# Kernel tuning notes

Measured on AMD Instinct MI355X. Metric: run time of the kernel, lower is better.

Reference implementation:

```python
import jax, jax.numpy as jnp
import numpy as np

N_NODES = 100000
N_EDGES = 3200000
IN_DIM = 256
HIDDEN = 128
OUT_DIM = 64


def setup_inputs() -> dict:
    key = jax.random.key(0)
    k = jax.random.split(key, 6)
    x = jax.random.normal(k[0], (N_NODES, IN_DIM), dtype=jnp.float32)
    adj_vals = jax.random.uniform(k[1], (N_EDGES,), dtype=jnp.float32)
    # glorot init as in the original
    s1 = np.sqrt(6.0 / (IN_DIM + HIDDEN)).astype(np.float32)
    s2 = np.sqrt(6.0 / (HIDDEN + OUT_DIM)).astype(np.float32)
    w1 = jax.random.uniform(k[2], (IN_DIM, HIDDEN), dtype=jnp.float32, minval=-s1, maxval=s1)
    w2 = jax.random.uniform(k[3], (HIDDEN, OUT_DIM), dtype=jnp.float32, minval=-s2, maxval=s2)
    edge_src = jax.random.randint(k[4], (N_EDGES,), 0, N_NODES, dtype=jnp.int32)
    edge_dst = jax.random.randint(k[5], (N_EDGES,), 0, N_NODES, dtype=jnp.int32)
    return {"x": x, "adj_vals": adj_vals, "w1": w1, "w2": w2,
            "edge_src": edge_src, "edge_dst": edge_dst}


def _spmm(adj_vals, edge_src, edge_dst, h, n_nodes):
    """Sparse adjacency (COO) times dense matrix: out[d] = sum_e vals[e]*h[src[e]]."""
    msgs = adj_vals[:, None] * h[edge_src]  # [E, D] gather + scale
    return jax.ops.segment_sum(msgs, edge_dst, num_segments=n_nodes)


def reference(x, adj_vals, w1, w2, edge_src, edge_dst):
    # Layer 1: pre_sup = X @ W1; support = A @ pre_sup; relu
    h = jax.nn.relu(_spmm(adj_vals, edge_src, edge_dst, x @ w1, N_NODES))
    # Layer 2: identity activation -> logits
    logits = _spmm(adj_vals, edge_src, edge_dst, h @ w2, N_NODES)
    return logits
```

## Files before the change

### kernel.cpp

```cpp
#include <hip/hip_runtime.h>

#define N_NODES 100000
#define N_EDGES 3200000
#define IN_DIM 256
#define HIDDEN 128
#define OUT_DIM 64

#define NBUCK 782
#define CHUNK 5120
#define BCAP 6144

typedef unsigned int uint32;
typedef unsigned short ushort16;

typedef short short8 __attribute__((ext_vector_type(8)));
typedef float f32x4 __attribute__((ext_vector_type(4)));

__device__ __forceinline__ ushort16 f2bf(float f) {
    uint32 u = __float_as_uint(f);
    u += 0x7fffu + ((u >> 16) & 1u);
    return (ushort16)(u >> 16);
}

__device__ __forceinline__ void splitbf(float f, unsigned short& hi, unsigned short& lo) {
    uint32 u = __float_as_uint(f);
    uint32 r = u + 0x7fffu + ((u >> 16) & 1u);
    hi = (unsigned short)(r >> 16);
    float hf = __uint_as_float((r >> 16) << 16);
    float res = f - hf;
    uint32 v = __float_as_uint(res);
    lo = (unsigned short)((v + 0x7fffu + ((v >> 16) & 1u)) >> 16);
}


__global__ __launch_bounds__(256)
void hist_bucket(const int* __restrict__ edst, int* __restrict__ bcnt, int E) {
    __shared__ int h[NBUCK];
    for (int b = threadIdx.x; b < NBUCK; b += 256) h[b] = 0;
    __syncthreads();
    for (int i = blockIdx.x * 256 + threadIdx.x; i < E; i += gridDim.x * 256)
        atomicAdd(&h[edst[i] >> 7], 1);
    __syncthreads();
    for (int b = threadIdx.x; b < NBUCK; b += 256) {
        int c = h[b];
        if (c) atomicAdd(&bcnt[b], c);
    }
}


__global__ __launch_bounds__(256)
void bucket_scan(const int* __restrict__ bcnt, int* __restrict__ bptr,
                 int* __restrict__ cursor, int* __restrict__ row_ptr, int E) {
    __shared__ int st[256];
    int tid = threadIdx.x;
    int v4[4];
    int s0 = 0;
#pragma unroll
    for (int k = 0; k < 4; k++) {
        int b = tid * 4 + k;
        v4[k] = (b < NBUCK) ? bcnt[b] : 0;
        s0 += v4[k];
    }
    st[tid] = s0;
    __syncthreads();
    for (int off = 1; off < 256; off <<= 1) {
        int t = (tid >= off) ? st[tid - off] : 0;
        __syncthreads();
        st[tid] += t;
        __syncthreads();
    }
    int run = st[tid] - s0;
#pragma unroll
    for (int k = 0; k < 4; k++) {
        int b = tid * 4 + k;
        if (b < NBUCK) { bptr[b] = run; cursor[b] = run; }
        run += v4[k];
    }
    if (tid == 255) bptr[NBUCK] = run;
    if (tid == 0) row_ptr[N_NODES] = E;
}


__global__ __launch_bounds__(256)
void partition_kernel(const int* __restrict__ esrc, const int* __restrict__ edst,
                      const float* __restrict__ evals, int* __restrict__ cursor,
                      int2* __restrict__ part, int E) {
    __shared__ int hist[NBUCK];
    __shared__ int basepos[NBUCK];
    __shared__ int st[256];
    __shared__ unsigned short sbb[CHUNK];
    __shared__ int2 sbp[CHUNK];
    int tid = threadIdx.x;
    long base = (long)blockIdx.x * CHUNK;
    int cnt = (int)min((long)CHUNK, (long)E - base);

    for (int b = tid; b < NBUCK; b += 256) hist[b] = 0;
    __syncthreads();
    for (int j = tid; j < cnt; j += 256)
        atomicAdd(&hist[edst[base + j] >> 7], 1);
    __syncthreads();

    int v4[4];
    int s0 = 0;
#pragma unroll
    for (int k = 0; k < 4; k++) {
        int b = tid * 4 + k;
        v4[k] = (b < NBUCK) ? hist[b] : 0;
        s0 += v4[k];
    }
    st[tid] = s0;
    __syncthreads();
    for (int off = 1; off < 256; off <<= 1) {
        int t = (tid >= off) ? st[tid - off] : 0;
        __syncthreads();
        st[tid] += t;
        __syncthreads();
    }
    int run = st[tid] - s0;
#pragma unroll
    for (int k = 0; k < 4; k++) {
        int b = tid * 4 + k;
        if (b < NBUCK) {
            int gbase = (v4[k] > 0) ? atomicAdd(&cursor[b], v4[k]) : 0;
            basepos[b] = gbase - run;
            hist[b] = run;
        }
        run += v4[k];
    }
    __syncthreads();

    for (int j = tid; j < cnt; j += 256) {
        int d = edst[base + j];
        int b = d >> 7;
        int pos = atomicAdd(&hist[b], 1);
        sbb[pos] = (unsigned short)b;
        sbp[pos] = make_int2(esrc[base + j] | ((d & 127) << 17),
                             __float_as_int(evals[base + j]));
    }
    __syncthreads();

    for (int j = tid; j < cnt; j += 256) {
        int b = sbb[j];
        part[basepos[b] + j] = sbp[j];
    }
}


__global__ __launch_bounds__(256)
void bucket_to_csr(const int* __restrict__ bptr, int2* __restrict__ part,
                   int* __restrict__ row_ptr) {
    __shared__ int2 se[BCAP];
    __shared__ int rcnt[128];
    __shared__ int rcur[128];
    int tid = threadIdx.x;
    int b = blockIdx.x;
    int s = bptr[b], e = bptr[b + 1];
    int cnt = min(e - s, BCAP);

    if (tid < 128) rcnt[tid] = 0;
    __syncthreads();
    for (int j = tid; j < cnt; j += 256) {
        int2 p = part[s + j];
        se[j] = p;
        atomicAdd(&rcnt[p.x >> 17], 1);
    }
    __syncthreads();

    int v = (tid < 128) ? rcnt[tid] : 0;
    if (tid < 128) rcur[tid] = v;
    __syncthreads();
    for (int off = 1; off < 128; off <<= 1) {
        int t = 0;
        if (tid < 128 && tid >= off) t = rcur[tid - off];
        __syncthreads();
        if (tid < 128 && tid >= off) rcur[tid] += t;
        __syncthreads();
    }
    if (tid < 128) {
        int excl = rcur[tid] - v;
        rcur[tid] = excl;
        int row = b * 128 + tid;
        if (row < N_NODES) row_ptr[row] = s + excl;
    }
    __syncthreads();

    for (int j = tid; j < cnt; j += 256) {
        int2 p = se[j];
        int r = p.x >> 17;
        int pos = atomicAdd(&rcur[r], 1);
        part[s + pos] = make_int2(p.x & 0x1FFFF, p.y);
    }
}


__global__ __launch_bounds__(256)
void splitw_kernel(const float* __restrict__ w1, const float* __restrict__ w2,
                   ushort16* __restrict__ w1t_hi, ushort16* __restrict__ w1t_lo,
                   ushort16* __restrict__ w2t_hi, ushort16* __restrict__ w2t_lo) {
    int g = blockIdx.x * 256 + threadIdx.x;
    if (g < IN_DIM * HIDDEN) {
        int k = g / HIDDEN, n = g % HIDDEN;
        unsigned short h, l;
        splitbf(w1[g], h, l);
        w1t_hi[n * IN_DIM + k] = h;
        w1t_lo[n * IN_DIM + k] = l;
    } else {
        int g2 = g - IN_DIM * HIDDEN;
        if (g2 < HIDDEN * OUT_DIM) {
            int k = g2 / OUT_DIM, n = g2 % OUT_DIM;
            unsigned short h, l;
            splitbf(w2[g2], h, l);
            w2t_hi[n * HIDDEN + k] = h;
            w2t_lo[n * HIDDEN + k] = l;
        }
    }
}


template <int K, int BN>
__launch_bounds__(256)
__global__ void gemm_mfma(const float* __restrict__ A,
                          const ushort16* __restrict__ Bt_hi,
                          const ushort16* __restrict__ Bt_lo,
                          ushort16* __restrict__ C, int M) {
    constexpr int BM = 128, BK = 64;
    constexpr int NF = BN / 32;
    __shared__ __align__(16) unsigned short Ah[BM * BK];
    __shared__ __align__(16) unsigned short Al[BM * BK];

    int tid = threadIdx.x;
    int wid = tid >> 6, lane = tid & 63;
    int wr = wid >> 1, wc = wid & 1;
    int rowBase = blockIdx.x * BM;
    int r = lane & 15, kg = lane >> 4;
    int swzmask = (lane & 7) << 4;

    f32x4 zero = {0.f, 0.f, 0.f, 0.f};
    f32x4 acc[4][NF];
#pragma unroll
    for (int m = 0; m < 4; m++)
#pragma unroll
        for (int n = 0; n < NF; n++) acc[m][n] = zero;

    int sk4 = (tid & 15) * 4;
    int sm0 = tid >> 4;

    for (int k0 = 0; k0 < K; k0 += BK) {
#pragma unroll
        for (int i = 0; i < 8; i++) {
            int m = sm0 + i * 16;
            int row = rowBase + m;
            float4 f = make_float4(0.f, 0.f, 0.f, 0.f);
            if (row < M) f = *(const float4*)(A + (size_t)row * K + k0 + sk4);
            ushort4 h, l;
            splitbf(f.x, h.x, l.x);
            splitbf(f.y, h.y, l.y);
            splitbf(f.z, h.z, l.z);
            splitbf(f.w, h.w, l.w);
            int bo = (m * BK + sk4) * 2;
            int swz = bo ^ ((m & 7) << 4);
            *(ushort4*)((char*)Ah + swz) = h;
            *(ushort4*)((char*)Al + swz) = l;
        }
        __syncthreads();

#pragma unroll
        for (int kk = 0; kk < BK / 32; kk++) {
            short8 ah[4], al[4];
            int abase = (wr * 64 + r) * (BK * 2) + kk * 64 + kg * 16;
#pragma unroll
            for (int m = 0; m < 4; m++) {
                int swz = (abase + m * (16 * BK * 2)) ^ swzmask;
                ah[m] = *(const short8*)((const char*)Ah + swz);
                al[m] = *(const short8*)((const char*)Al + swz);
            }
            short8 bh[NF], bl[NF];
#pragma unroll
            for (int n = 0; n < NF; n++) {
                size_t off = (size_t)(wc * (BN / 2) + n * 16 + r) * K + k0 + kk * 32 + kg * 8;
                bh[n] = *(const short8*)(Bt_hi + off);
                bl[n] = *(const short8*)(Bt_lo + off);
            }
#pragma unroll
            for (int m = 0; m < 4; m++)
#pragma unroll
                for (int n = 0; n < NF; n++) {
                    acc[m][n] = __builtin_amdgcn_mfma_f32_16x16x32_bf16(ah[m], bh[n], acc[m][n], 0, 0, 0);
                    acc[m][n] = __builtin_amdgcn_mfma_f32_16x16x32_bf16(ah[m], bl[n], acc[m][n], 0, 0, 0);
                    acc[m][n] = __builtin_amdgcn_mfma_f32_16x16x32_bf16(al[m], bh[n], acc[m][n], 0, 0, 0);
                }
        }
        __syncthreads();
    }

#pragma unroll
    for (int m = 0; m < 4; m++) {
        int row0 = rowBase + wr * 64 + m * 16 + kg * 4;
#pragma unroll
        for (int j = 0; j < 4; j++) {
            int row = row0 + j;
            if (row < M) {
#pragma unroll
                for (int n = 0; n < NF; n++) {
                    int col = wc * (BN / 2) + n * 16 + r;
                    C[(size_t)row * BN + col] = f2bf(acc[m][n][j]);
                }
            }
        }
    }
}


template <int D, bool RELU>
__launch_bounds__(256)
__global__ void spmm_kernel(const ushort16* __restrict__ feat, const int2* __restrict__ csr_pair,
                            const int* __restrict__ row_ptr, float* __restrict__ out, int n) {
    constexpr int LPR = D * 2 / 16;
    constexpr int EPG = 64 / LPR;
    int wid = threadIdx.x >> 6;
    int lane = threadIdx.x & 63;
    int row = blockIdx.x * 4 + wid;
    if (row >= n) return;
    int s = row_ptr[row], e = row_ptr[row + 1];

    int sub = lane / LPR;
    int slot = lane % LPR;
    const char* fbase = (const char*)feat + slot * 16;

    float acc[8];
#pragma unroll
    for (int j = 0; j < 8; j++) acc[j] = 0.f;

    for (int i = s; i < e; i += 2 * EPG) {
        int i0 = i + sub;
        int i1 = i + EPG + sub;
        int2 p0 = csr_pair[min(i0, e - 1)];
        int2 p1 = csr_pair[min(i1, e - 1)];
        float v0 = (i0 < e) ? __int_as_float(p0.y) : 0.f;
        float v1 = (i1 < e) ? __int_as_float(p1.y) : 0.f;
        uint4 u0 = *(const uint4*)(fbase + (size_t)p0.x * (D * 2));
        uint4 u1 = *(const uint4*)(fbase + (size_t)p1.x * (D * 2));
#pragma unroll
        for (int t = 0; t < 4; t++) {
            uint32 w0 = (&u0.x)[t];
            acc[2 * t]     += v0 * __uint_as_float(w0 << 16);
            acc[2 * t + 1] += v0 * __uint_as_float(w0 & 0xffff0000u);
        }
#pragma unroll
        for (int t = 0; t < 4; t++) {
            uint32 w1 = (&u1.x)[t];
            acc[2 * t]     += v1 * __uint_as_float(w1 << 16);
            acc[2 * t + 1] += v1 * __uint_as_float(w1 & 0xffff0000u);
        }
    }

#pragma unroll
    for (int m = LPR; m < 64; m <<= 1) {
#pragma unroll
        for (int j = 0; j < 8; j++) acc[j] += __shfl_xor(acc[j], m);
    }

    if (RELU) {
#pragma unroll
        for (int j = 0; j < 8; j++) acc[j] = acc[j] > 0.f ? acc[j] : 0.f;
    }

    if (lane < LPR) {
        float4* o = (float4*)(out + (size_t)row * D + slot * 8);
        o[0] = make_float4(acc[0], acc[1], acc[2], acc[3]);
        o[1] = make_float4(acc[4], acc[5], acc[6], acc[7]);
    }
}


extern "C" void kernel_launch(void* const* d_in, const int* in_sizes, int n_in,
                              void* d_out, int out_size, void* d_ws, size_t ws_size,
                              hipStream_t stream) {
    const float* x    = (const float*)d_in[0];
    const float* adj  = (const float*)d_in[1];
    const float* w1   = (const float*)d_in[2];
    const float* w2   = (const float*)d_in[3];
    const int*   esrc = (const int*)d_in[4];
    const int*   edst = (const int*)d_in[5];
    float* out = (float*)d_out;

    const int N = N_NODES;
    const int E = N_EDGES;

    char* ws = (char*)d_ws;
    size_t off = 0;
    auto take = [&](size_t bytes) -> char* {
        char* p = ws + off;
        off = (off + bytes + 255) & ~(size_t)255;
        return p;
    };
    int*      bcnt    = (int*)take((size_t)NBUCK * 4);
    int*      bptr    = (int*)take((size_t)(NBUCK + 1) * 4);
    int*      cursor  = (int*)take((size_t)NBUCK * 4);
    int*      row_ptr = (int*)take((size_t)(N + 1) * 4);
    int2*     part    = (int2*)take((size_t)E * 8);
    ushort16* pre1    = (ushort16*)take((size_t)N * HIDDEN * 2);
    ushort16* pre2    = (ushort16*)take((size_t)N * OUT_DIM * 2);
    float*    h       = (float*)take((size_t)N * HIDDEN * 4);
    ushort16* w1t_hi  = (ushort16*)take((size_t)HIDDEN * IN_DIM * 2);
    ushort16* w1t_lo  = (ushort16*)take((size_t)HIDDEN * IN_DIM * 2);
    ushort16* w2t_hi  = (ushort16*)take((size_t)OUT_DIM * HIDDEN * 2);
    ushort16* w2t_lo  = (ushort16*)take((size_t)OUT_DIM * HIDDEN * 2);

    splitw_kernel<<<(IN_DIM * HIDDEN + HIDDEN * OUT_DIM + 255) / 256, 256, 0, stream>>>(
        w1, w2, w1t_hi, w1t_lo, w2t_hi, w2t_lo);

    hipMemsetAsync(bcnt, 0, (size_t)NBUCK * 4, stream);
    hist_bucket<<<1024, 256, 0, stream>>>(edst, bcnt, E);
    bucket_scan<<<1, 256, 0, stream>>>(bcnt, bptr, cursor, row_ptr, E);
    partition_kernel<<<(E + CHUNK - 1) / CHUNK, 256, 0, stream>>>(esrc, edst, adj, cursor, part, E);
    bucket_to_csr<<<NBUCK, 256, 0, stream>>>(bptr, part, row_ptr);

    gemm_mfma<IN_DIM, HIDDEN><<<(N + 127) / 128, 256, 0, stream>>>(x, w1t_hi, w1t_lo, pre1, N);
    spmm_kernel<HIDDEN, true><<<(N + 3) / 4, 256, 0, stream>>>(pre1, part, row_ptr, h, N);

    gemm_mfma<HIDDEN, OUT_DIM><<<(N + 127) / 128, 256, 0, stream>>>(h, w2t_hi, w2t_lo, pre2, N);
    spmm_kernel<OUT_DIM, false><<<(N + 3) / 4, 256, 0, stream>>>(pre2, part, row_ptr, out, N);
}
```

Measured before the change: 579.4 us.

## Fuse layer-1 SpMM with ReLU and layer-2 GEMM; pre-swizzle weights to fragment order

Adds a fused kernel in which each 512-thread block aggregates 128 rows of the layer-1 SpMM, applies ReLU, splits the result into bf16 hi/lo in LDS, and multiplies by W2 with MFMA to write pre2 directly. This removes the fp32 hidden-matrix round trip through global memory and one kernel launch. The weight prep kernel now writes W1 and W2 in MFMA fragment order so B loads become contiguous per lane. In exchange the fused kernel uses 64KB of LDS with large blocks, which lowers occupancy for the latency-bound gather phase.

```diff
diff --git a/kernel.cpp b/kernel.cpp
--- a/kernel.cpp
+++ b/kernel.cpp
@@ -195,23 +195,39 @@
 
 __global__ __launch_bounds__(256)
 void splitw_kernel(const float* __restrict__ w1, const float* __restrict__ w2,
-                   ushort16* __restrict__ w1t_hi, ushort16* __restrict__ w1t_lo,
-                   ushort16* __restrict__ w2t_hi, ushort16* __restrict__ w2t_lo) {
+                   unsigned short* __restrict__ w1f_hi, unsigned short* __restrict__ w1f_lo,
+                   unsigned short* __restrict__ w2f_hi, unsigned short* __restrict__ w2f_lo) {
+    const int W1_SLOTS = (IN_DIM / 32) * (HIDDEN / 16) * 64;
+    const int W2_SLOTS = (HIDDEN / 32) * (OUT_DIM / 16) * 64;
     int g = blockIdx.x * 256 + threadIdx.x;
-    if (g < IN_DIM * HIDDEN) {
-        int k = g / HIDDEN, n = g % HIDDEN;
-        unsigned short h, l;
-        splitbf(w1[g], h, l);
-        w1t_hi[n * IN_DIM + k] = h;
-        w1t_lo[n * IN_DIM + k] = l;
-    } else {
-        int g2 = g - IN_DIM * HIDDEN;
-        if (g2 < HIDDEN * OUT_DIM) {
-            int k = g2 / OUT_DIM, n = g2 % OUT_DIM;
+    if (g < W1_SLOTS) {
+        int lane = g & 63;
+        int rest = g >> 6;
+        int nfrag = rest & 7;
+        int kblk = rest >> 3;
+        int n = nfrag * 16 + (lane & 15);
+        int k0 = kblk * 32 + (lane >> 4) * 8;
+#pragma unroll
+        for (int j = 0; j < 8; j++) {
             unsigned short h, l;
-            splitbf(w2[g2], h, l);
-            w2t_hi[n * HIDDEN + k] = h;
-            w2t_lo[n * HIDDEN + k] = l;
+            splitbf(w1[(size_t)(k0 + j) * HIDDEN + n], h, l);
+            w1f_hi[(size_t)g * 8 + j] = h;
+            w1f_lo[(size_t)g * 8 + j] = l;
+        }
+    } else if (g < W1_SLOTS + W2_SLOTS) {
+        int g2 = g - W1_SLOTS;
+        int lane = g2 & 63;
+        int rest = g2 >> 6;
+        int nfrag = rest & 3;
+        int kblk = rest >> 2;
+        int n = nfrag * 16 + (lane & 15);
+        int k0 = kblk * 32 + (lane >> 4) * 8;
+#pragma unroll
+        for (int j = 0; j < 8; j++) {
+            unsigned short h, l;
+            splitbf(w2[(size_t)(k0 + j) * OUT_DIM + n], h, l);
+            w2f_hi[(size_t)g2 * 8 + j] = h;
+            w2f_lo[(size_t)g2 * 8 + j] = l;
         }
     }
 }
@@ -220,8 +236,8 @@
 template <int K, int BN>
 __launch_bounds__(256)
 __global__ void gemm_mfma(const float* __restrict__ A,
-                          const ushort16* __restrict__ Bt_hi,
-                          const ushort16* __restrict__ Bt_lo,
+                          const unsigned short* __restrict__ Bf_hi,
+                          const unsigned short* __restrict__ Bf_lo,
                           ushort16* __restrict__ C, int M) {
     constexpr int BM = 128, BK = 64;
     constexpr int NF = BN / 32;
@@ -275,11 +291,13 @@
                 al[m] = *(const short8*)((const char*)Al + swz);
             }
             short8 bh[NF], bl[NF];
+            int kblk = (k0 >> 5) + kk;
 #pragma unroll
             for (int n = 0; n < NF; n++) {
-                size_t off = (size_t)(wc * (BN / 2) + n * 16 + r) * K + k0 + kk * 32 + kg * 8;
-                bh[n] = *(const short8*)(Bt_hi + off);
-                bl[n] = *(const short8*)(Bt_lo + off);
+                int nf = wc * NF + n;
+                size_t off = ((size_t)(kblk * (BN / 16) + nf) * 64 + lane) * 8;
+                bh[n] = *(const short8*)(Bf_hi + off);
+                bl[n] = *(const short8*)(Bf_lo + off);
             }
 #pragma unroll
             for (int m = 0; m < 4; m++)
@@ -306,6 +324,113 @@
                     C[(size_t)row * BN + col] = f2bf(acc[m][n][j]);
                 }
             }
+        }
+    }
+}
+
+
+__launch_bounds__(512)
+__global__ void spmm_gemm_fused(const ushort16* __restrict__ feat, const int2* __restrict__ csr_pair,
+                                const int* __restrict__ row_ptr,
+                                const unsigned short* __restrict__ w2f_hi,
+                                const unsigned short* __restrict__ w2f_lo,
+                                ushort16* __restrict__ pre2, int n) {
+    __shared__ __align__(16) unsigned short Hh[128 * 128];
+    __shared__ __align__(16) unsigned short Hl[128 * 128];
+    int tid = threadIdx.x;
+    int wid = tid >> 6;
+    int lane = tid & 63;
+    int sub = lane >> 4;
+    int slot = lane & 15;
+    int bucket = blockIdx.x;
+    const char* fbase = (const char*)feat + slot * 16;
+
+    for (int rl = 0; rl < 16; rl++) {
+        int lrow = wid * 16 + rl;
+        int row = bucket * 128 + lrow;
+        int s = 0, e = 0;
+        if (row < n) { s = row_ptr[row]; e = row_ptr[row + 1]; }
+        float acc0[8];
+#pragma unroll
+        for (int j = 0; j < 8; j++) acc0[j] = 0.f;
+
+        for (int i = s; i < e; i += 16) {
+            int2 pp[4]; float vv[4]; uint4 uu[4];
+#pragma unroll
+            for (int q = 0; q < 4; q++) {
+                int ii = i + q * 4 + sub;
+                pp[q] = csr_pair[min(ii, e - 1)];
+                vv[q] = (ii < e) ? __int_as_float(pp[q].y) : 0.f;
+            }
+#pragma unroll
+            for (int q = 0; q < 4; q++)
+                uu[q] = *(const uint4*)(fbase + (size_t)pp[q].x * 256);
+#pragma unroll
+            for (int q = 0; q < 4; q++) {
+#pragma unroll
+                for (int t = 0; t < 4; t++) {
+                    uint32 w = (&uu[q].x)[t];
+                    acc0[2 * t]     += vv[q] * __uint_as_float(w << 16);
+                    acc0[2 * t + 1] += vv[q] * __uint_as_float(w & 0xffff0000u);
+                }
+            }
+        }
+
+#pragma unroll
+        for (int m = 16; m < 64; m <<= 1) {
+#pragma unroll
+            for (int j = 0; j < 8; j++) acc0[j] += __shfl_xor(acc0[j], m);
+        }
+
+        if (lane < 16) {
+            short8 hv, lv;
+#pragma unroll
+            for (int j = 0; j < 8; j++) {
+                float a = acc0[j] > 0.f ? acc0[j] : 0.f;
+                unsigned short hh, ll;
+                splitbf(a, hh, ll);
+                hv[j] = (short)hh;
+                lv[j] = (short)ll;
+            }
+            int bo = lrow * 256 + slot * 16;
+            int swz = bo ^ ((lrow & 7) << 4);
+            *(short8*)((char*)Hh + swz) = hv;
+            *(short8*)((char*)Hl + swz) = lv;
+        }
+    }
+    __syncthreads();
+
+    int r = lane & 15, kg = lane >> 4;
+    int lrow2 = wid * 16 + r;
+    f32x4 zero = {0.f, 0.f, 0.f, 0.f};
+    f32x4 acc2[4];
+#pragma unroll
+    for (int nn = 0; nn < 4; nn++) acc2[nn] = zero;
+
+#pragma unroll
+    for (int kk = 0; kk < 4; kk++) {
+        int bo = lrow2 * 256 + kk * 64 + kg * 16;
+        int swz = bo ^ ((lrow2 & 7) << 4);
+        short8 ah = *(const short8*)((const char*)Hh + swz);
+        short8 al = *(const short8*)((const char*)Hl + swz);
+#pragma unroll
+        for (int nn = 0; nn < 4; nn++) {
+            size_t off = ((size_t)(kk * 4 + nn) * 64 + lane) * 8;
+            short8 bh = *(const short8*)(w2f_hi + off);
+            short8 bl = *(const short8*)(w2f_lo + off);
+            acc2[nn] = __builtin_amdgcn_mfma_f32_16x16x32_bf16(ah, bh, acc2[nn], 0, 0, 0);
+            acc2[nn] = __builtin_amdgcn_mfma_f32_16x16x32_bf16(ah, bl, acc2[nn], 0, 0, 0);
+            acc2[nn] = __builtin_amdgcn_mfma_f32_16x16x32_bf16(al, bh, acc2[nn], 0, 0, 0);
+        }
+    }
+
+#pragma unroll
+    for (int j = 0; j < 4; j++) {
+        int row = bucket * 128 + wid * 16 + kg * 4 + j;
+        if (row < n) {
+#pragma unroll
+            for (int nn = 0; nn < 4; nn++)
+                pre2[(size_t)row * OUT_DIM + nn * 16 + r] = f2bf(acc2[nn][j]);
         }
     }
 }
@@ -401,14 +526,12 @@
     int2*     part    = (int2*)take((size_t)E * 8);
     ushort16* pre1    = (ushort16*)take((size_t)N * HIDDEN * 2);
     ushort16* pre2    = (ushort16*)take((size_t)N * OUT_DIM * 2);
-    float*    h       = (float*)take((size_t)N * HIDDEN * 4);
-    ushort16* w1t_hi  = (ushort16*)take((size_t)HIDDEN * IN_DIM * 2);
-    ushort16* w1t_lo  = (ushort16*)take((size_t)HIDDEN * IN_DIM * 2);
-    ushort16* w2t_hi  = (ushort16*)take((size_t)OUT_DIM * HIDDEN * 2);
-    ushort16* w2t_lo  = (ushort16*)take((size_t)OUT_DIM * HIDDEN * 2);
-
-    splitw_kernel<<<(IN_DIM * HIDDEN + HIDDEN * OUT_DIM + 255) / 256, 256, 0, stream>>>(
-        w1, w2, w1t_hi, w1t_lo, w2t_hi, w2t_lo);
+    unsigned short* w1f_hi = (unsigned short*)take((size_t)HIDDEN * IN_DIM * 2);
+    unsigned short* w1f_lo = (unsigned short*)take((size_t)HIDDEN * IN_DIM * 2);
+    unsigned short* w2f_hi = (unsigned short*)take((size_t)OUT_DIM * HIDDEN * 2);
+    unsigned short* w2f_lo = (unsigned short*)take((size_t)OUT_DIM * HIDDEN * 2);
+
+    splitw_kernel<<<20, 256, 0, stream>>>(w1, w2, w1f_hi, w1f_lo, w2f_hi, w2f_lo);
 
     hipMemsetAsync(bcnt, 0, (size_t)NBUCK * 4, stream);
     hist_bucket<<<1024, 256, 0, stream>>>(edst, bcnt, E);
@@ -416,9 +539,9 @@
     partition_kernel<<<(E + CHUNK - 1) / CHUNK, 256, 0, stream>>>(esrc, edst, adj, cursor, part, E);
     bucket_to_csr<<<NBUCK, 256, 0, stream>>>(bptr, part, row_ptr);
 
-    gemm_mfma<IN_DIM, HIDDEN><<<(N + 127) / 128, 256, 0, stream>>>(x, w1t_hi, w1t_lo, pre1, N);
-    spmm_kernel<HIDDEN, true><<<(N + 3) / 4, 256, 0, stream>>>(pre1, part, row_ptr, h, N);
-
-    gemm_mfma<HIDDEN, OUT_DIM><<<(N + 127) / 128, 256, 0, stream>>>(h, w2t_hi, w2t_lo, pre2, N);
+    gemm_mfma<IN_DIM, HIDDEN><<<(N + 127) / 128, 256, 0, stream>>>(x, w1f_hi, w1f_lo, pre1, N);
+
+    spmm_gemm_fused<<<NBUCK, 512, 0, stream>>>(pre1, part, row_ptr, w2f_hi, w2f_lo, pre2, N);
+
     spmm_kernel<OUT_DIM, false><<<(N + 3) / 4, 256, 0, stream>>>(pre2, part, row_ptr, out, N);
 }
```

Result: no change. 569.7 us (-1.7%).

## Pre-swizzle weights into MFMA fragment order and unroll SpMM gathers by four

Applied to the files above, without the earlier changes.

The weight-split kernel now writes W1/W2 hi/lo halves directly in per-lane MFMA fragment order, so each lane in the GEMM loads its B fragment with one contiguous 16-byte read instead of a strided transposed access. Separately, the SpMM inner loop issues four independent edge/feature gathers per iteration instead of two, to keep more memory loads in flight. The wider unroll raises register use and wastes more clamped loads on short rows.

```diff
diff --git a/kernel.cpp b/kernel.cpp
--- a/kernel.cpp
+++ b/kernel.cpp
@@ -195,23 +195,39 @@
 
 __global__ __launch_bounds__(256)
 void splitw_kernel(const float* __restrict__ w1, const float* __restrict__ w2,
-                   ushort16* __restrict__ w1t_hi, ushort16* __restrict__ w1t_lo,
-                   ushort16* __restrict__ w2t_hi, ushort16* __restrict__ w2t_lo) {
+                   unsigned short* __restrict__ w1f_hi, unsigned short* __restrict__ w1f_lo,
+                   unsigned short* __restrict__ w2f_hi, unsigned short* __restrict__ w2f_lo) {
+    const int W1_SLOTS = (IN_DIM / 32) * (HIDDEN / 16) * 64;
+    const int W2_SLOTS = (HIDDEN / 32) * (OUT_DIM / 16) * 64;
     int g = blockIdx.x * 256 + threadIdx.x;
-    if (g < IN_DIM * HIDDEN) {
-        int k = g / HIDDEN, n = g % HIDDEN;
-        unsigned short h, l;
-        splitbf(w1[g], h, l);
-        w1t_hi[n * IN_DIM + k] = h;
-        w1t_lo[n * IN_DIM + k] = l;
-    } else {
-        int g2 = g - IN_DIM * HIDDEN;
-        if (g2 < HIDDEN * OUT_DIM) {
-            int k = g2 / OUT_DIM, n = g2 % OUT_DIM;
+    if (g < W1_SLOTS) {
+        int lane = g & 63;
+        int rest = g >> 6;
+        int nfrag = rest & 7;
+        int kblk = rest >> 3;
+        int n = nfrag * 16 + (lane & 15);
+        int k0 = kblk * 32 + (lane >> 4) * 8;
+#pragma unroll
+        for (int j = 0; j < 8; j++) {
             unsigned short h, l;
-            splitbf(w2[g2], h, l);
-            w2t_hi[n * HIDDEN + k] = h;
-            w2t_lo[n * HIDDEN + k] = l;
+            splitbf(w1[(size_t)(k0 + j) * HIDDEN + n], h, l);
+            w1f_hi[(size_t)g * 8 + j] = h;
+            w1f_lo[(size_t)g * 8 + j] = l;
+        }
+    } else if (g < W1_SLOTS + W2_SLOTS) {
+        int g2 = g - W1_SLOTS;
+        int lane = g2 & 63;
+        int rest = g2 >> 6;
+        int nfrag = rest & 3;
+        int kblk = rest >> 2;
+        int n = nfrag * 16 + (lane & 15);
+        int k0 = kblk * 32 + (lane >> 4) * 8;
+#pragma unroll
+        for (int j = 0; j < 8; j++) {
+            unsigned short h, l;
+            splitbf(w2[(size_t)(k0 + j) * OUT_DIM + n], h, l);
+            w2f_hi[(size_t)g2 * 8 + j] = h;
+            w2f_lo[(size_t)g2 * 8 + j] = l;
         }
     }
 }
@@ -220,8 +236,8 @@
 template <int K, int BN>
 __launch_bounds__(256)
 __global__ void gemm_mfma(const float* __restrict__ A,
-                          const ushort16* __restrict__ Bt_hi,
-                          const ushort16* __restrict__ Bt_lo,
+                          const unsigned short* __restrict__ Bf_hi,
+                          const unsigned short* __restrict__ Bf_lo,
                           ushort16* __restrict__ C, int M) {
     constexpr int BM = 128, BK = 64;
     constexpr int NF = BN / 32;
@@ -275,11 +291,13 @@
                 al[m] = *(const short8*)((const char*)Al + swz);
             }
             short8 bh[NF], bl[NF];
+            int kblk = (k0 >> 5) + kk;
 #pragma unroll
             for (int n = 0; n < NF; n++) {
-                size_t off = (size_t)(wc * (BN / 2) + n * 16 + r) * K + k0 + kk * 32 + kg * 8;
-                bh[n] = *(const short8*)(Bt_hi + off);
-                bl[n] = *(const short8*)(Bt_lo + off);
+                int nf = wc * NF + n;
+                size_t off = ((size_t)(kblk * (BN / 16) + nf) * 64 + lane) * 8;
+                bh[n] = *(const short8*)(Bf_hi + off);
+                bl[n] = *(const short8*)(Bf_lo + off);
             }
 #pragma unroll
             for (int m = 0; m < 4; m++)
@@ -331,26 +349,25 @@
 #pragma unroll
     for (int j = 0; j < 8; j++) acc[j] = 0.f;
 
-    for (int i = s; i < e; i += 2 * EPG) {
-        int i0 = i + sub;
-        int i1 = i + EPG + sub;
-        int2 p0 = csr_pair[min(i0, e - 1)];
-        int2 p1 = csr_pair[min(i1, e - 1)];
-        float v0 = (i0 < e) ? __int_as_float(p0.y) : 0.f;
-        float v1 = (i1 < e) ? __int_as_float(p1.y) : 0.f;
-        uint4 u0 = *(const uint4*)(fbase + (size_t)p0.x * (D * 2));
-        uint4 u1 = *(const uint4*)(fbase + (size_t)p1.x * (D * 2));
-#pragma unroll
-        for (int t = 0; t < 4; t++) {
-            uint32 w0 = (&u0.x)[t];
-            acc[2 * t]     += v0 * __uint_as_float(w0 << 16);
-            acc[2 * t + 1] += v0 * __uint_as_float(w0 & 0xffff0000u);
-        }
-#pragma unroll
-        for (int t = 0; t < 4; t++) {
-            uint32 w1 = (&u1.x)[t];
-            acc[2 * t]     += v1 * __uint_as_float(w1 << 16);
-            acc[2 * t + 1] += v1 * __uint_as_float(w1 & 0xffff0000u);
+    for (int i = s; i < e; i += 4 * EPG) {
+        int2 p[4]; float v[4]; uint4 u[4];
+#pragma unroll
+        for (int q = 0; q < 4; q++) {
+            int ii = i + q * EPG + sub;
+            p[q] = csr_pair[min(ii, e - 1)];
+            v[q] = (ii < e) ? __int_as_float(p[q].y) : 0.f;
+        }
+#pragma unroll
+        for (int q = 0; q < 4; q++)
+            u[q] = *(const uint4*)(fbase + (size_t)p[q].x * (D * 2));
+#pragma unroll
+        for (int q = 0; q < 4; q++) {
+#pragma unroll
+            for (int t = 0; t < 4; t++) {
+                uint32 w = (&u[q].x)[t];
+                acc[2 * t]     += v[q] * __uint_as_float(w << 16);
+                acc[2 * t + 1] += v[q] * __uint_as_float(w & 0xffff0000u);
+            }
         }
     }
 
@@ -402,13 +419,12 @@
     ushort16* pre1    = (ushort16*)take((size_t)N * HIDDEN * 2);
     ushort16* pre2    = (ushort16*)take((size_t)N * OUT_DIM * 2);
     float*    h       = (float*)take((size_t)N * HIDDEN * 4);
-    ushort16* w1t_hi  = (ushort16*)take((size_t)HIDDEN * IN_DIM * 2);
-    ushort16* w1t_lo  = (ushort16*)take((size_t)HIDDEN * IN_DIM * 2);
-    ushort16* w2t_hi  = (ushort16*)take((size_t)OUT_DIM * HIDDEN * 2);
-    ushort16* w2t_lo  = (ushort16*)take((size_t)OUT_DIM * HIDDEN * 2);
-
-    splitw_kernel<<<(IN_DIM * HIDDEN + HIDDEN * OUT_DIM + 255) / 256, 256, 0, stream>>>(
-        w1, w2, w1t_hi, w1t_lo, w2t_hi, w2t_lo);
+    unsigned short* w1f_hi = (unsigned short*)take((size_t)HIDDEN * IN_DIM * 2);
+    unsigned short* w1f_lo = (unsigned short*)take((size_t)HIDDEN * IN_DIM * 2);
+    unsigned short* w2f_hi = (unsigned short*)take((size_t)OUT_DIM * HIDDEN * 2);
+    unsigned short* w2f_lo = (unsigned short*)take((size_t)OUT_DIM * HIDDEN * 2);
+
+    splitw_kernel<<<20, 256, 0, stream>>>(w1, w2, w1f_hi, w1f_lo, w2f_hi, w2f_lo);
 
     hipMemsetAsync(bcnt, 0, (size_t)NBUCK * 4, stream);
     hist_bucket<<<1024, 256, 0, stream>>>(edst, bcnt, E);
@@ -416,9 +432,9 @@
     partition_kernel<<<(E + CHUNK - 1) / CHUNK, 256, 0, stream>>>(esrc, edst, adj, cursor, part, E);
     bucket_to_csr<<<NBUCK, 256, 0, stream>>>(bptr, part, row_ptr);
 
-    gemm_mfma<IN_DIM, HIDDEN><<<(N + 127) / 128, 256, 0, stream>>>(x, w1t_hi, w1t_lo, pre1, N);
+    gemm_mfma<IN_DIM, HIDDEN><<<(N + 127) / 128, 256, 0, stream>>>(x, w1f_hi, w1f_lo, pre1, N);
     spmm_kernel<HIDDEN, true><<<(N + 3) / 4, 256, 0, stream>>>(pre1, part, row_ptr, h, N);
 
-    gemm_mfma<HIDDEN, OUT_DIM><<<(N + 127) / 128, 256, 0, stream>>>(h, w2t_hi, w2t_lo, pre2, N);
+    gemm_mfma<HIDDEN, OUT_DIM><<<(N + 127) / 128, 256, 0, stream>>>(h, w2f_hi, w2f_lo, pre2, N);
     spmm_kernel<OUT_DIM, false><<<(N + 3) / 4, 256, 0, stream>>>(pre2, part, row_ptr, out, N);
 }
```

Result: faster. 549.0 us (-5.3%).
